# Performance work log

Hardware: AMD Instinct MI355X
Metric: run time of the kernel (lower is better)

Reference implementation:

```python
import jax, jax.numpy as jnp
import numpy as np

N_E = 1024
E_DIM = 256
BETA = 0.25
EMA_LAMBDA = 0.99

def setup_inputs() -> dict:
    key = jax.random.key(0)
    k1, k2 = jax.random.split(key)
    z = jax.random.normal(k1, (32, 2048, E_DIM), dtype=jnp.float32)
    # torch init: uniform(-1/n_e, 1/n_e)
    embedding = jax.random.uniform(k2, (N_E, E_DIM), dtype=jnp.float32,
                                   minval=-1.0 / N_E, maxval=1.0 / N_E)
    N_t = jnp.zeros((N_E,), dtype=jnp.float32)
    m_t = jnp.zeros((N_E, E_DIM), dtype=jnp.float32)
    return {"z": z, "embedding": embedding, "N_t": N_t, "m_t": m_t}

def reference(z, embedding, N_t, m_t):
    zf = z.reshape(-1, E_DIM)  # [N, e_dim]
    # squared L2 distances: ||z||^2 + ||e||^2 - 2 z e^T  -> [N, n_e]
    d = (jnp.sum(zf * zf, axis=1, keepdims=True)
         + jnp.sum(embedding * embedding, axis=1)
         - 2.0 * jnp.matmul(zf, embedding.T))
    idx = jnp.argmin(d, axis=1)  # [N] int

    # EMA statistics (torch does a python loop over unique indices; this is the
    # vectorized equivalent: only codes that were selected get updated).
    counts = jax.ops.segment_sum(jnp.ones_like(idx, dtype=jnp.float32), idx, num_segments=N_E)
    sums = jax.ops.segment_sum(zf, idx, num_segments=N_E)  # [n_e, e_dim]
    selected = counts > 0
    N_t_new = jnp.where(selected, N_t * EMA_LAMBDA + counts * (1.0 - EMA_LAMBDA), N_t)
    m_t_new = jnp.where(selected[:, None], m_t * EMA_LAMBDA + sums * (1.0 - EMA_LAMBDA), m_t)

    z_q = embedding[idx].reshape(z.shape)
    loss = BETA * jnp.mean((jax.lax.stop_gradient(z_q) - z) ** 2)
    z_q_st = z + jax.lax.stop_gradient(z_q - z)  # straight-through

    # perplexity from code usage histogram (== mean of one-hot encodings)
    e_mean = counts / idx.shape[0]
    perplexity = jnp.exp(-jnp.sum(e_mean * jnp.log(e_mean + 1e-10)))
    return (loss, z_q_st, idx, perplexity, N_t_new, m_t_new)
```

## Files before the change

kernel.cpp:

```cpp
#include <hip/hip_runtime.h>
#include <math.h>

#define N_ROWS  65536
#define EDIM    256
#define NE      1024
#define BETA    0.25f
#define LAMBDA  0.99f

#define MARGIN  8e-3f
#define QCAP    2048


#define O_ZQ   1
#define O_IDX  16777217
#define O_PERP 16842753
#define O_NT   16842754
#define O_MT   16843778

typedef __attribute__((ext_vector_type(8))) short short8;
typedef __attribute__((ext_vector_type(4))) float f32x4;

__device__ __forceinline__ unsigned short f2bf(float f) {
    unsigned u = __float_as_uint(f);
    return (unsigned short)((u + 0x7fffu + ((u >> 16) & 1u)) >> 16);
}

__global__ __launch_bounds__(64) void prep_b_kernel(const float* __restrict__ emb,
                                                    unsigned* __restrict__ bfrag_u32,
                                                    float* __restrict__ loss_acc,
                                                    int* __restrict__ cnt) {
    int j = blockIdx.x;
    int l = threadIdx.x;
    float4 v = ((const float4*)(emb + (size_t)j * EDIM))[l];
    unsigned lo = (unsigned)f2bf(v.x) | ((unsigned)f2bf(v.y) << 16);
    unsigned hi = (unsigned)f2bf(v.z) | ((unsigned)f2bf(v.w) << 16);
    int base = ((((j >> 4) * 8 + (l >> 3)) * 64) + ((l >> 1) & 3) * 16 + (j & 15)) * 4
             + 2 * (l & 1);
    bfrag_u32[base]     = lo;
    bfrag_u32[base + 1] = hi;
    if (l == 0) cnt[j] = 0;
    if (j == 0 && l == 0) *loss_acc = 0.0f;
}

__global__ __launch_bounds__(256) void sq_kernel(const float* __restrict__ src,
                                                 float* __restrict__ dst) {
    const int tid = threadIdx.x;
    const int grp = tid >> 4;
    const int q   = tid & 15;
    const int row = blockIdx.x * 16 + grp;
    const int h = q >> 3, j = q & 7;
    const float* __restrict__ p = src + (size_t)row * EDIM + h * 128 + j;
    float acc = __fmul_rn(p[0], p[0]);
    #pragma unroll
    for (int t = 1; t < 16; ++t) {
        float v = p[8 * t];
        acc = __fadd_rn(acc, __fmul_rn(v, v));
    }
    acc = __fadd_rn(acc, __shfl_xor(acc, 1));
    acc = __fadd_rn(acc, __shfl_xor(acc, 2));
    acc = __fadd_rn(acc, __shfl_xor(acc, 4));
    acc = __fadd_rn(acc, __shfl_xor(acc, 8));
    if (q == 0) dst[row] = acc;
}

__global__ __launch_bounds__(256, 3) void argmin_kernel(const float* __restrict__ z,
                                                        const float* __restrict__ emb,
                                                        const short8* __restrict__ bfrag,
                                                        const float* __restrict__ e_sq,
                                                        int* __restrict__ idx_out,
                                                        float* __restrict__ out_zq,
                                                        float* __restrict__ out_idx,
                                                        float* __restrict__ loss_acc,
                                                        int* __restrict__ cnt) {
    __shared__ float e_lds[NE];
    __shared__ uint2 queue[QCAP];
    __shared__ unsigned long long best_s[32];
    __shared__ float rmW_s[4][32];
    __shared__ float rmF_s[32];
    __shared__ float zsq_s[32];
    __shared__ int   idx_s[32];
    __shared__ int   qcnt;

    const int tid = threadIdx.x;
    const int wid = tid >> 6, lane = tid & 63;
    const int l15 = lane & 15, lg = lane >> 4;
    const int row0 = blockIdx.x * 32;

    if (tid < 32) best_s[tid] = ~0ull;
    if (tid == 0) qcnt = 0;
    #pragma unroll
    for (int i = 0; i < 4; ++i) e_lds[tid + 256 * i] = e_sq[tid + 256 * i];

    short8 a[2][8];
    #pragma unroll
    for (int rt = 0; rt < 2; ++rt) {
        float zs = 0.f;
        #pragma unroll
        for (int ks = 0; ks < 8; ++ks) {
            const float* zp = z + (size_t)(row0 + rt * 16 + l15) * EDIM + ks * 32 + lg * 8;
            float4 f0 = *(const float4*)zp;
            float4 f1 = *(const float4*)(zp + 4);
            zs += f0.x * f0.x + f0.y * f0.y + f0.z * f0.z + f0.w * f0.w
                + f1.x * f1.x + f1.y * f1.y + f1.z * f1.z + f1.w * f1.w;
            union { short8 s; unsigned short u[8]; } pk;
            pk.u[0] = f2bf(f0.x); pk.u[1] = f2bf(f0.y); pk.u[2] = f2bf(f0.z); pk.u[3] = f2bf(f0.w);
            pk.u[4] = f2bf(f1.x); pk.u[5] = f2bf(f1.y); pk.u[6] = f2bf(f1.z); pk.u[7] = f2bf(f1.w);
            a[rt][ks] = pk.s;
        }
        zs += __shfl_xor(zs, 16);
        zs += __shfl_xor(zs, 32);
        if (wid == rt && lg == 0) zsq_s[rt * 16 + l15] = zs;
    }

    float rm[2] = {1e30f, 1e30f};
    __syncthreads();

    for (int ch = 0; ch < 16; ++ch) {
        const int cb = wid * 256 + ch * 16;
        short8 b[8];
        #pragma unroll
        for (int ks = 0; ks < 8; ++ks)
            b[ks] = bfrag[((size_t)(wid * 16 + ch) * 8 + ks) * 64 + lane];

        f32x4 acc[2];
        #pragma unroll
        for (int rt = 0; rt < 2; ++rt) acc[rt] = (f32x4){0.f, 0.f, 0.f, 0.f};
        #pragma unroll
        for (int ks = 0; ks < 8; ++ks)
            #pragma unroll
            for (int rt = 0; rt < 2; ++rt)
                acc[rt] = __builtin_amdgcn_mfma_f32_16x16x32_bf16(b[ks], a[rt][ks], acc[rt], 0, 0, 0);

        const float4 eq = ((const float4*)e_lds)[(cb >> 2) + lg];

        #pragma unroll
        for (int rt = 0; rt < 2; ++rt) {
            float t0 = __fsub_rn(eq.x, __fmul_rn(2.0f, acc[rt][0]));
            float t1 = __fsub_rn(eq.y, __fmul_rn(2.0f, acc[rt][1]));
            float t2 = __fsub_rn(eq.z, __fmul_rn(2.0f, acc[rt][2]));
            float t3 = __fsub_rn(eq.w, __fmul_rn(2.0f, acc[rt][3]));
            float m = fminf(fminf(t0, t1), fminf(t2, t3));
            m = fminf(m, __shfl_xor(m, 16));
            m = fminf(m, __shfl_xor(m, 32));
            rm[rt] = fminf(rm[rt], m);
            const float thr = rm[rt] + MARGIN;
            const int rl = rt * 16 + l15;
            if (t0 <= thr) { int s = atomicAdd(&qcnt, 1); if (s < QCAP) queue[s] = make_uint2((rl << 10) | (cb + lg * 4 + 0), __float_as_uint(t0)); }
            if (t1 <= thr) { int s = atomicAdd(&qcnt, 1); if (s < QCAP) queue[s] = make_uint2((rl << 10) | (cb + lg * 4 + 1), __float_as_uint(t1)); }
            if (t2 <= thr) { int s = atomicAdd(&qcnt, 1); if (s < QCAP) queue[s] = make_uint2((rl << 10) | (cb + lg * 4 + 2), __float_as_uint(t2)); }
            if (t3 <= thr) { int s = atomicAdd(&qcnt, 1); if (s < QCAP) queue[s] = make_uint2((rl << 10) | (cb + lg * 4 + 3), __float_as_uint(t3)); }
        }
    }

    if (lg == 0) {
        rmW_s[wid][l15]      = rm[0];
        rmW_s[wid][16 + l15] = rm[1];
    }
    __syncthreads();
    if (tid < 32)
        rmF_s[tid] = fminf(fminf(rmW_s[0][tid], rmW_s[1][tid]),
                           fminf(rmW_s[2][tid], rmW_s[3][tid]));
    __syncthreads();

    {
        int nq = qcnt; if (nq > QCAP) nq = QCAP;
        const int g = tid >> 3, q = tid & 7;
        for (int e = g; e < nq; e += 32) {
            uint2 ent = queue[e];
            int rl = ent.x >> 10, col = ent.x & 1023;
            if (__uint_as_float(ent.y) > rmF_s[rl] + MARGIN) continue;
            const float4* zr = (const float4*)(z + (size_t)(row0 + rl) * EDIM);
            const float4* er = (const float4*)(emb + (size_t)col * EDIM);
            float ae = 0.f;
            #pragma unroll
            for (int i = 0; i < 8; ++i) {
                float4 x = zr[q + 8 * i], y = er[q + 8 * i];
                ae = __fmaf_rn(x.x, y.x, ae);
                ae = __fmaf_rn(x.y, y.y, ae);
                ae = __fmaf_rn(x.z, y.z, ae);
                ae = __fmaf_rn(x.w, y.w, ae);
            }
            ae = __fadd_rn(ae, __shfl_xor(ae, 1));
            ae = __fadd_rn(ae, __shfl_xor(ae, 2));
            ae = __fadd_rn(ae, __shfl_xor(ae, 4));
            if (q == 0) {
                float d = __fsub_rn(__fadd_rn(zsq_s[rl], e_lds[col]), __fmul_rn(2.0f, ae));
                unsigned u = __float_as_uint(d);
                u = (u & 0x80000000u) ? ~u : (u | 0x80000000u);
                unsigned long long key = ((unsigned long long)u << 32) | (unsigned)col;
                atomicMin(&best_s[rl], key);
            }
        }
    }

    __syncthreads();
    if (tid < 32) {
        unsigned long long k = best_s[tid];
        int id = (int)(k & 1023u);
        idx_out[row0 + tid] = id;
        out_idx[row0 + tid] = (float)id;
        idx_s[tid] = id;
        atomicAdd(&cnt[id], 1);
    }
    __syncthreads();

    const float4* e4 = (const float4*)emb;
    #pragma unroll
    for (int i = 0; i < 8; ++i) {
        int flat = tid + i * 256;
        int r = flat >> 6, c4 = flat & 63;
        int id = idx_s[r];
        float4 e = e4[(size_t)id * 64 + c4];
        float* o = out_zq + (size_t)(row0 + r) * EDIM + c4 * 4;
        o[0] = e.x; o[1] = e.y; o[2] = e.z; o[3] = e.w;
    }

    if (wid == 0) {
        float lp = 0.f;
        if (lane < 32) {
            unsigned m = (unsigned)(best_s[lane] >> 32);
            unsigned bits = (m & 0x80000000u) ? (m & 0x7fffffffu) : ~m;
            lp = __uint_as_float(bits);
        }
        #pragma unroll
        for (int mm = 32; mm; mm >>= 1) lp += __shfl_down(lp, mm);
        if (lane == 0) atomicAdd(loss_acc, lp);
    }
}

__global__ __launch_bounds__(1024) void scan_kernel(const int* __restrict__ cnt,
                                                    const float* __restrict__ N_t,
                                                    float* __restrict__ outN,
                                                    float* __restrict__ counts_f,
                                                    int* __restrict__ offs,
                                                    int* __restrict__ cursor) {
    __shared__ int s[1024];
    const int tid = threadIdx.x;
    int c = cnt[tid];
    s[tid] = c;
    __syncthreads();
    for (int d = 1; d < 1024; d <<= 1) {
        int v = (tid >= d) ? s[tid - d] : 0;
        __syncthreads();
        s[tid] += v;
        __syncthreads();
    }
    int excl = s[tid] - c;
    offs[tid] = excl;
    cursor[tid] = excl;
    counts_f[tid] = (float)c;
    float Nold = N_t[tid];
    outN[tid] = (c > 0) ? Nold * LAMBDA + (float)c * (1.0f - LAMBDA) : Nold;
}

__global__ __launch_bounds__(256) void scatter_kernel(const int* __restrict__ idx,
                                                      int* __restrict__ cursor,
                                                      int* __restrict__ sorted) {
    int i = blockIdx.x * 256 + threadIdx.x;
    int p = atomicAdd(&cursor[idx[i]], 1);
    sorted[p] = i;
}

__global__ __launch_bounds__(512) void msum_kernel(const float* __restrict__ z,
                                                   const int* __restrict__ sorted,
                                                   const int* __restrict__ offs,
                                                   const int* __restrict__ cnt,
                                                   const float* __restrict__ m_t,
                                                   float* __restrict__ outM) {
    const int j = blockIdx.x;
    const int tid = threadIdx.x, w = tid >> 6, lane = tid & 63;
    const int n = cnt[j], start = offs[j];
    float4 acc = make_float4(0.f, 0.f, 0.f, 0.f);
    for (int e = w; e < n; e += 8) {
        float4 v = ((const float4*)(z + (size_t)sorted[start + e] * EDIM))[lane];
        acc.x += v.x; acc.y += v.y; acc.z += v.z; acc.w += v.w;
    }
    __shared__ float red[8 * 256];
    *(float4*)(red + w * 256 + lane * 4) = acc;
    __syncthreads();
    if (tid < 256) {
        float s = 0.f;
        #pragma unroll
        for (int ww = 0; ww < 8; ++ww) s += red[ww * 256 + tid];
        float mold = m_t[(size_t)j * EDIM + tid];
        outM[(size_t)j * EDIM + tid] = (n > 0) ? mold * LAMBDA + s * (1.0f - LAMBDA) : mold;
    }
}

__global__ __launch_bounds__(256) void final_kernel(const float* __restrict__ counts,
                                                    const float* __restrict__ loss_acc,
                                                    float* __restrict__ out_loss,
                                                    float* __restrict__ out_perp) {
    const int tid = threadIdx.x, w = tid >> 6, lane = tid & 63;
    float h = 0.f;
    for (int c = tid; c < NE; c += 256) {
        float em = counts[c] * (1.0f / (float)N_ROWS);
        h += em * logf(em + 1e-10f);
    }
    #pragma unroll
    for (int m = 32; m; m >>= 1) h += __shfl_down(h, m);
    __shared__ float red[4];
    if (lane == 0) red[w] = h;
    __syncthreads();
    if (tid == 0) {
        float H = red[0] + red[1] + red[2] + red[3];
        out_perp[0] = expf(-H);
        out_loss[0] = BETA * loss_acc[0] * (1.0f / (float)(N_ROWS * EDIM));
    }
}

extern "C" void kernel_launch(void* const* d_in, const int* in_sizes, int n_in,
                              void* d_out, int out_size, void* d_ws, size_t ws_size,
                              hipStream_t stream) {
    const float* z   = (const float*)d_in[0];
    const float* emb = (const float*)d_in[1];
    const float* N_t = (const float*)d_in[2];
    const float* m_t = (const float*)d_in[3];
    float* out = (float*)d_out;
    float* ws  = (float*)d_ws;

    float* loss_acc   = ws;
    float* e_sq       = ws + 64;
    unsigned* bfrag_u = (unsigned*)(ws + 67584);
    int*   sorted     = (int*)(ws + 198656);
    int*   idx1       = (int*)(ws + 264192);
    float* counts     = ws + 329728;
    int*   cnt_i      = (int*)(ws + 330752);
    int*   offs_i     = (int*)(ws + 331776);
    int*   cursor_i   = (int*)(ws + 332800);

    prep_b_kernel<<<NE, 64, 0, stream>>>(emb, bfrag_u, loss_acc, cnt_i);
    sq_kernel<<<NE / 16, 256, 0, stream>>>(emb, e_sq);
    argmin_kernel<<<N_ROWS / 32, 256, 0, stream>>>(z, emb, (const short8*)bfrag_u,
                                                   e_sq, idx1,
                                                   out + O_ZQ, out + O_IDX, loss_acc, cnt_i);
    scan_kernel<<<1, 1024, 0, stream>>>(cnt_i, N_t, out + O_NT, counts, offs_i, cursor_i);
    scatter_kernel<<<N_ROWS / 256, 256, 0, stream>>>(idx1, cursor_i, sorted);
    msum_kernel<<<NE, 512, 0, stream>>>(z, sorted, offs_i, cnt_i, m_t, out + O_MT);
    final_kernel<<<1, 256, 0, stream>>>(counts, loss_acc, out, out + O_PERP);
}
```

Measured before the change: 318.9 us.

## Split A-fragment loading across waves via LDS and double-buffer codebook fragments

Each wave now converts only a quarter of the z tile to bf16 and stages it in shared memory, instead of every wave redundantly loading and converting the full 32-row tile. Squared norms are combined from per-wave partial sums. The codebook B fragments are double-buffered so the global loads for the next chunk are in flight while the current chunk's MFMAs and filtering run. The distance computation is also fused into a single FMA. The costs are extra LDS, an extra barrier, and more live registers for the second B buffer, which may reduce occupancy.

```diff
diff --git a/kernel.cpp b/kernel.cpp
--- a/kernel.cpp
+++ b/kernel.cpp
@@ -72,11 +72,13 @@
                                                         float* __restrict__ out_idx,
                                                         float* __restrict__ loss_acc,
                                                         int* __restrict__ cnt) {
+    __shared__ __align__(16) uint4 A_stg[16 * 64];
     __shared__ float e_lds[NE];
     __shared__ uint2 queue[QCAP];
     __shared__ unsigned long long best_s[32];
     __shared__ float rmW_s[4][32];
     __shared__ float rmF_s[32];
+    __shared__ float zsqP[4][16];
     __shared__ float zsq_s[32];
     __shared__ int   idx_s[32];
     __shared__ int   qcnt;
@@ -91,54 +93,67 @@
     #pragma unroll
     for (int i = 0; i < 4; ++i) e_lds[tid + 256 * i] = e_sq[tid + 256 * i];
 
-    short8 a[2][8];
-    #pragma unroll
-    for (int rt = 0; rt < 2; ++rt) {
+    {
         float zs = 0.f;
         #pragma unroll
-        for (int ks = 0; ks < 8; ++ks) {
+        for (int i = 0; i < 4; ++i) {
+            const int p  = wid * 4 + i;
+            const int rt = p >> 3, ks = p & 7;
             const float* zp = z + (size_t)(row0 + rt * 16 + l15) * EDIM + ks * 32 + lg * 8;
             float4 f0 = *(const float4*)zp;
             float4 f1 = *(const float4*)(zp + 4);
             zs += f0.x * f0.x + f0.y * f0.y + f0.z * f0.z + f0.w * f0.w
                 + f1.x * f1.x + f1.y * f1.y + f1.z * f1.z + f1.w * f1.w;
-            union { short8 s; unsigned short u[8]; } pk;
+            union { short8 s; unsigned short u[8]; uint4 q; } pk;
             pk.u[0] = f2bf(f0.x); pk.u[1] = f2bf(f0.y); pk.u[2] = f2bf(f0.z); pk.u[3] = f2bf(f0.w);
             pk.u[4] = f2bf(f1.x); pk.u[5] = f2bf(f1.y); pk.u[6] = f2bf(f1.z); pk.u[7] = f2bf(f1.w);
-            a[rt][ks] = pk.s;
+            A_stg[p * 64 + lane] = pk.q;
         }
         zs += __shfl_xor(zs, 16);
         zs += __shfl_xor(zs, 32);
-        if (wid == rt && lg == 0) zsq_s[rt * 16 + l15] = zs;
-    }
+        if (lg == 0) zsqP[wid][l15] = zs;
+    }
+
+    const short8* bp = bfrag + (size_t)wid * 8192;
+    short8 bA[8], bB[8];
+    #pragma unroll
+    for (int ks = 0; ks < 8; ++ks) bA[ks] = bp[ks * 64 + lane];
+
+    __syncthreads();
+
+    if (tid < 32) {
+        int rt = tid >> 4, r = tid & 15;
+        zsq_s[tid] = zsqP[rt * 2][r] + zsqP[rt * 2 + 1][r];
+    }
+
+    short8 a[2][8];
+    #pragma unroll
+    for (int rt = 0; rt < 2; ++rt)
+        #pragma unroll
+        for (int ks = 0; ks < 8; ++ks) {
+            uint4 q = A_stg[(rt * 8 + ks) * 64 + lane];
+            a[rt][ks] = *(short8*)&q;
+        }
 
     float rm[2] = {1e30f, 1e30f};
-    __syncthreads();
-
-    for (int ch = 0; ch < 16; ++ch) {
+
+    auto FILTER = [&](int ch, short8* b) {
+        f32x4 acc[2];
+        acc[0] = (f32x4){0.f, 0.f, 0.f, 0.f};
+        acc[1] = (f32x4){0.f, 0.f, 0.f, 0.f};
+        #pragma unroll
+        for (int ks = 0; ks < 8; ++ks) {
+            acc[0] = __builtin_amdgcn_mfma_f32_16x16x32_bf16(b[ks], a[0][ks], acc[0], 0, 0, 0);
+            acc[1] = __builtin_amdgcn_mfma_f32_16x16x32_bf16(b[ks], a[1][ks], acc[1], 0, 0, 0);
+        }
         const int cb = wid * 256 + ch * 16;
-        short8 b[8];
-        #pragma unroll
-        for (int ks = 0; ks < 8; ++ks)
-            b[ks] = bfrag[((size_t)(wid * 16 + ch) * 8 + ks) * 64 + lane];
-
-        f32x4 acc[2];
-        #pragma unroll
-        for (int rt = 0; rt < 2; ++rt) acc[rt] = (f32x4){0.f, 0.f, 0.f, 0.f};
-        #pragma unroll
-        for (int ks = 0; ks < 8; ++ks)
-            #pragma unroll
-            for (int rt = 0; rt < 2; ++rt)
-                acc[rt] = __builtin_amdgcn_mfma_f32_16x16x32_bf16(b[ks], a[rt][ks], acc[rt], 0, 0, 0);
-
         const float4 eq = ((const float4*)e_lds)[(cb >> 2) + lg];
-
         #pragma unroll
         for (int rt = 0; rt < 2; ++rt) {
-            float t0 = __fsub_rn(eq.x, __fmul_rn(2.0f, acc[rt][0]));
-            float t1 = __fsub_rn(eq.y, __fmul_rn(2.0f, acc[rt][1]));
-            float t2 = __fsub_rn(eq.z, __fmul_rn(2.0f, acc[rt][2]));
-            float t3 = __fsub_rn(eq.w, __fmul_rn(2.0f, acc[rt][3]));
+            float t0 = __fmaf_rn(-2.0f, acc[rt][0], eq.x);
+            float t1 = __fmaf_rn(-2.0f, acc[rt][1], eq.y);
+            float t2 = __fmaf_rn(-2.0f, acc[rt][2], eq.z);
+            float t3 = __fmaf_rn(-2.0f, acc[rt][3], eq.w);
             float m = fminf(fminf(t0, t1), fminf(t2, t3));
             m = fminf(m, __shfl_xor(m, 16));
             m = fminf(m, __shfl_xor(m, 32));
@@ -150,6 +165,17 @@
             if (t2 <= thr) { int s = atomicAdd(&qcnt, 1); if (s < QCAP) queue[s] = make_uint2((rl << 10) | (cb + lg * 4 + 2), __float_as_uint(t2)); }
             if (t3 <= thr) { int s = atomicAdd(&qcnt, 1); if (s < QCAP) queue[s] = make_uint2((rl << 10) | (cb + lg * 4 + 3), __float_as_uint(t3)); }
         }
+    };
+
+    for (int ch = 0; ch < 16; ch += 2) {
+        #pragma unroll
+        for (int ks = 0; ks < 8; ++ks) bB[ks] = bp[((ch + 1) * 8 + ks) * 64 + lane];
+        FILTER(ch, bA);
+        if (ch + 2 < 16) {
+            #pragma unroll
+            for (int ks = 0; ks < 8; ++ks) bA[ks] = bp[((ch + 2) * 8 + ks) * 64 + lane];
+        }
+        FILTER(ch + 1, bB);
     }
 
     if (lg == 0) {
```

After: 300.4 us. -5.8%, faster.
